# Kernel tuning notes

Hardware: AMD Instinct MI355X
Metric: run time of the kernel (lower is better)

The kernel has to match this reference:

```python
import jax, jax.numpy as jnp
import numpy as np
import math

B, NV, L = 64, 21, 2048
PATCH, STRIDE = 16, 8
PNUM = (L - PATCH) // STRIDE + 1  # 255 patches
D, H, NDIM = 128, 256, 2
PRED = 96
EPS = 1e-5
SCALE = 1.0 / math.sqrt(NDIM)  # MultiHeadEMA scale = sqrt(1/ndim)
# patch gather indices: [PNUM, PATCH]
PIDX = np.arange(PNUM)[:, None] * STRIDE + np.arange(PATCH)[None, :]


def setup_inputs() -> dict:
    key = jax.random.key(0)
    ks = jax.random.split(key, 24)
    nrm = lambda k, shape, std: std * jax.random.normal(k, shape, jnp.float32)
    inp = {}
    inp['x'] = jax.random.normal(ks[0], (B, NV, L), jnp.float32)
    # LEMencoder feature_projection: LEMblock(PATCH -> H -> D)
    inp['fp_w1'] = nrm(ks[1], (PATCH, H), 0.1)
    inp['fp_b1'] = jnp.zeros((H,), jnp.float32)
    inp['fp_w2'] = nrm(ks[2], (H, D), 0.1)
    inp['fp_b2'] = jnp.zeros((D,), jnp.float32)
    inp['fp_wr'] = nrm(ks[3], (PATCH, D), 0.1)
    inp['fp_br'] = jnp.zeros((D,), jnp.float32)
    inp['fp_g'] = jnp.ones((D,), jnp.float32)
    inp['fp_be'] = jnp.zeros((D,), jnp.float32)
    # 2 stacked encoder LEMblocks (D -> D -> D), leading layer axis
    inp['enc_w1'] = nrm(ks[4], (2, D, D), 0.05)
    inp['enc_b1'] = jnp.zeros((2, D), jnp.float32)
    inp['enc_w2'] = nrm(ks[5], (2, D, D), 0.05)
    inp['enc_b2'] = jnp.zeros((2, D), jnp.float32)
    inp['enc_wr'] = nrm(ks[6], (2, D, D), 0.05)
    inp['enc_br'] = jnp.zeros((2, D), jnp.float32)
    inp['enc_g'] = jnp.ones((2, D), jnp.float32)
    inp['enc_be'] = jnp.zeros((2, D), jnp.float32)
    # MultiHeadEMA params (unidirectional: kernel_dim == D)
    inp['ema_delta'] = nrm(ks[7], (D, NDIM, 1), 0.2)
    inp['ema_alpha'] = nrm(ks[8], (D, NDIM, 1), 0.2)
    val = jnp.array([1.0, -1.0], jnp.float32).reshape(1, NDIM, 1)  # +1/-1 alternating init
    inp['ema_beta'] = nrm(ks[9], (D, NDIM, 1), 0.02) + val
    inp['ema_gamma'] = nrm(ks[10], (D, NDIM), 1.0)
    inp['ema_omega'] = nrm(ks[11], (D,), 1.0)
    # Flatten_Head (shared): Linear(D*PNUM -> PRED)
    inp['head_w'] = nrm(ks[12], (D * PNUM, PRED), 0.02)
    inp['head_b'] = jnp.zeros((PRED,), jnp.float32)
    return inp


def _lemblock(x, w1, b1, w2, b2, wr, br, g, be):
    h = jax.nn.relu(x @ w1 + b1) @ w2 + b2
    y = h + (x @ wr + br)
    mu = jnp.mean(y, axis=-1, keepdims=True)
    var = jnp.mean(jnp.square(y - mu), axis=-1, keepdims=True)
    return g * (y - mu) * jax.lax.rsqrt(var + EPS) + be


def reference(x, fp_w1, fp_b1, fp_w2, fp_b2, fp_wr, fp_br, fp_g, fp_be,
              enc_w1, enc_b1, enc_w2, enc_b2, enc_wr, enc_br, enc_g, enc_be,
              ema_delta, ema_alpha, ema_beta, ema_gamma, ema_omega,
              head_w, head_b):
    # patching: [B, NV, L] -> [B*NV, PNUM, PATCH]
    z = x[:, :, PIDX].reshape(B * NV, PNUM, PATCH)
    # LEMencoder
    z = _lemblock(z, fp_w1, fp_b1, fp_w2, fp_b2, fp_wr, fp_br, fp_g, fp_be)
    for i in range(enc_w1.shape[0]):
        z = _lemblock(z, enc_w1[i], enc_b1[i], enc_w2[i], enc_b2[i],
                      enc_wr[i], enc_br[i], enc_g[i], enc_be[i])
    # MultiHeadEMA over patch (time) axis; input [Time=PNUM, Batch=B*NV, Channel=D]
    t = jnp.transpose(z, (1, 0, 2))
    residual = t * ema_omega
    xc = jnp.transpose(t, (1, 2, 0))  # [BN, D, PNUM]
    p = jax.nn.sigmoid(ema_delta)           # [D, N, 1]
    q = 1.0 - p * jax.nn.sigmoid(ema_alpha)  # [D, N, 1]
    vander = jnp.arange(PNUM, dtype=jnp.float32)[None, None, :] * jnp.log(q)  # [D, N, PNUM]
    kern = p * ema_beta * jnp.exp(vander)
    k = jnp.einsum('dnl,dn->dl', kern, ema_gamma * SCALE)  # [D, PNUM]
    n2 = 2 * PNUM
    out = jnp.fft.irfft(jnp.fft.rfft(xc, n=n2) * jnp.fft.rfft(k, n=n2), n=n2)[..., :PNUM]
    out = jax.nn.silu(jnp.transpose(out, (2, 0, 1)) + residual)  # [PNUM, BN, D]
    # Flatten_Head (shared): [B, NV, D, PNUM] -> flatten(-2) -> linear
    u = jnp.transpose(out, (1, 2, 0)).reshape(B, NV, D * PNUM)
    return u @ head_w + head_b  # [B, NV, PRED]
```

## Files before the change

### kernel.cpp

```cpp
#include <hip/hip_runtime.h>

typedef unsigned short u16;
typedef short bf8v __attribute__((ext_vector_type(8)));
typedef float f4v __attribute__((ext_vector_type(4)));
typedef float f16v __attribute__((ext_vector_type(16)));

#define DEV static __device__ __forceinline__

constexpr int BB   = 64;
constexpr int NV   = 21;
constexpr int BN   = BB * NV;
constexpr int PNUM = 255;
constexpr int D    = 128;
constexpr int PRED = 96;
constexpr int ROWS = BN * PNUM;
constexpr int KH   = D * PNUM;
constexpr int CH   = 30;
constexpr int KPC  = KH / CH;
constexpr int HITER = KPC / 32;
constexpr float EMA_SCALE = 0.70710678118654752440f;

DEV float bf2f(u16 h) { return __uint_as_float(((unsigned)h) << 16); }
DEV u16 f2bf(float f) {
  unsigned u = __float_as_uint(f);
  return (u16)((u + 0x7fffu + ((u >> 16) & 1u)) >> 16);
}
DEV unsigned pkbf2(float a, float b) {
  unsigned ua = __float_as_uint(a) + 0x8000u;
  unsigned ub = __float_as_uint(b) + 0x8000u;
  return __builtin_amdgcn_perm(ub, ua, 0x07060302u);
}
DEV bf8v mk4(unsigned a, unsigned b, unsigned c, unsigned d) {
  int4 t = {(int)a, (int)b, (int)c, (int)d};
  bf8v r;
  __builtin_memcpy(&r, &t, 16);
  return r;
}
DEV bf8v ld8(const u16* p) {
  bf8v r;
  __builtin_memcpy(&r, p, 16);
  return r;
}
DEV f4v mfma16(bf8v a, bf8v b, f4v c) {
  return __builtin_amdgcn_mfma_f32_16x16x32_bf16(a, b, c, 0, 0, 0);
}
DEV f16v mfma32(bf8v a, bf8v b, f16v c) {
  return __builtin_amdgcn_mfma_f32_32x32x16_bf16(a, b, c, 0, 0, 0);
}
DEV f16v zero16() {
  f16v r;
#pragma unroll
  for (int i = 0; i < 16; i++) r[i] = 0.f;
  return r;
}

#define FRG(pk, ks)                                                            \
  mk4(pk[(ks) >> 1][2 * ((ks) & 1)][0], pk[(ks) >> 1][2 * ((ks) & 1)][1],      \
      pk[(ks) >> 1][2 * ((ks) & 1) + 1][0], pk[(ks) >> 1][2 * ((ks) & 1) + 1][1])

__global__ void swz_all(
    const float* __restrict__ fw1, const float* __restrict__ fw2,
    const float* __restrict__ fwr, const float* __restrict__ ew1,
    const float* __restrict__ ew2, const float* __restrict__ ewr,
    const float* __restrict__ hw, u16* __restrict__ wb, u16* __restrict__ wsh) {
  int b = blockIdx.x;
  if (b >= 560) {
    int i = (b - 560) * 256 + threadIdx.x;
    if (i >= KH * PRED) return;
    int kp = i / PRED, n = i - kp * PRED;
    int l = kp >> 7, d = kp & 127;
    wsh[((size_t)(kp >> 3) * PRED + n) * 8 + (kp & 7)] =
        f2bf(hw[(size_t)(d * PNUM + l) * PRED + n]);
    return;
  }
  const float* src; u16* dst; int K, N, Kp;
  if (b < 32)       { src = fw1; dst = wb;          K = 16;  N = 256; Kp = 32; }
  else if (b < 160) { b -= 32;  src = fw2; dst = wb + 8192;  K = 256; N = 128; Kp = 256; }
  else if (b < 176) { b -= 160; src = fwr; dst = wb + 40960; K = 16;  N = 128; Kp = 32; }
  else {
    int e = (b - 176) >> 6; b = (b - 176) & 63;
    int l = e / 3, w = e - 3 * l;
    const float* basep = (w == 0) ? ew1 : (w == 1) ? ew2 : ewr;
    src = basep + (size_t)l * 16384;
    dst = wb + 45056 + e * 16384;
    K = 128; N = 128; Kp = 128;
  }
  int i = b * 256 + threadIdx.x;
  if (i >= Kp * N) return;
  int k = i / N, n = i - k * N;
  int np = (n & ~12) | ((n & 4) << 1) | ((n & 8) >> 1);
  u16 v = (k < K) ? f2bf(src[(size_t)k * N + np]) : (u16)0;
  dst[((size_t)(k >> 3) * N + n) * 8 + (k & 7)] = v;
}

__global__ __launch_bounds__(128, 2) void k_lem(
    const float* __restrict__ x,
    const u16* __restrict__ ws1, const float* __restrict__ b1,
    const u16* __restrict__ ws2, const u16* __restrict__ wsr,
    const float* __restrict__ b2, const float* __restrict__ br,
    const float* __restrict__ g, const float* __restrict__ be,
    const u16* __restrict__ wse, const float* __restrict__ eb1,
    const float* __restrict__ eb2, const float* __restrict__ ebr,
    const float* __restrict__ eg, const float* __restrict__ ebe,
    u16* __restrict__ zout) {
  __shared__ __align__(16) u16 zst[64 * 132];
  const int t = threadIdx.x;
  const int lane = t & 63, w = t >> 6;
  const int hh = lane >> 5, r5 = lane & 31;
  const int tile = blockIdx.x;
  const int row = tile * 64 + w * 32 + r5;

  bf8v azv;
  {
    unsigned R = (unsigned)row;
    unsigned bn = R / 255u;
    unsigned p = R - bn * 255u;
    const float* px = x + (size_t)bn * 2048u + p * 8u + hh * 8;
    float4 v0 = *(const float4*)px;
    float4 v1 = *(const float4*)(px + 4);
    azv = mk4(pkbf2(v0.x, v0.y), pkbf2(v0.z, v0.w),
              pkbf2(v1.x, v1.y), pkbf2(v1.z, v1.w));
  }

  unsigned hpk[8][4][2];
  unsigned zpk[4][4][2];

#pragma unroll
  for (int half = 0; half < 2; half++) {
    f16v a[4];
#pragma unroll
    for (int gg = 0; gg < 4; gg++) {
      bf8v wf = ld8(ws1 + ((size_t)(hh * 256 + (half * 4 + gg) * 32 + r5)) * 8);
      a[gg] = mfma32(wf, azv, zero16());
    }
#pragma unroll
    for (int gg = 0; gg < 4; gg++)
#pragma unroll
      for (int wq = 0; wq < 4; wq++) {
        int c0 = (half * 4 + gg) * 32 + ((wq >> 1) << 4) + ((wq & 1) << 2) + (hh << 3);
        float4 bv = *(const float4*)(b1 + c0);
        float v0 = fmaxf(a[gg][wq * 4 + 0] + bv.x, 0.f);
        float v1 = fmaxf(a[gg][wq * 4 + 1] + bv.y, 0.f);
        float v2 = fmaxf(a[gg][wq * 4 + 2] + bv.z, 0.f);
        float v3 = fmaxf(a[gg][wq * 4 + 3] + bv.w, 0.f);
        hpk[half * 4 + gg][wq][0] = pkbf2(v0, v1);
        hpk[half * 4 + gg][wq][1] = pkbf2(v2, v3);
      }
  }

  f16v acc[4];
  {
    bf8v wq[3][4];
#pragma unroll
    for (int b = 0; b < 2; b++)
#pragma unroll
      for (int gg = 0; gg < 4; gg++)
        wq[b][gg] = ld8(ws2 + ((size_t)((2 * b + hh) * 128 + gg * 32 + r5)) * 8);
    {
      bf8v wr4[4];
#pragma unroll
      for (int gg = 0; gg < 4; gg++)
        wr4[gg] = ld8(wsr + ((size_t)(hh * 128 + gg * 32 + r5)) * 8);
#pragma unroll
      for (int gg = 0; gg < 4; gg++) acc[gg] = mfma32(wr4[gg], azv, zero16());
    }
#pragma unroll
    for (int u = 0; u < 16; u++) {
      if (u + 2 < 16) {
#pragma unroll
        for (int gg = 0; gg < 4; gg++)
          wq[(u + 2) % 3][gg] =
              ld8(ws2 + ((size_t)((2 * (u + 2) + hh) * 128 + gg * 32 + r5)) * 8);
      }
      bf8v bfr = FRG(hpk, u);
#pragma unroll
      for (int gg = 0; gg < 4; gg++) acc[gg] = mfma32(wq[u % 3][gg], bfr, acc[gg]);
    }
    float s = 0.f, s2 = 0.f;
#pragma unroll
    for (int gg = 0; gg < 4; gg++)
#pragma unroll
      for (int wq4 = 0; wq4 < 4; wq4++) {
        int c0 = gg * 32 + ((wq4 >> 1) << 4) + ((wq4 & 1) << 2) + (hh << 3);
        float4 bv2 = *(const float4*)(b2 + c0);
        float4 bvr = *(const float4*)(br + c0);
        acc[gg][wq4 * 4 + 0] += bv2.x + bvr.x;
        acc[gg][wq4 * 4 + 1] += bv2.y + bvr.y;
        acc[gg][wq4 * 4 + 2] += bv2.z + bvr.z;
        acc[gg][wq4 * 4 + 3] += bv2.w + bvr.w;
#pragma unroll
        for (int sidx = 0; sidx < 4; sidx++) {
          float v = acc[gg][wq4 * 4 + sidx];
          s += v; s2 += v * v;
        }
      }
    s += __shfl_xor(s, 32, 64); s2 += __shfl_xor(s2, 32, 64);
    float mean = s * (1.f / 128.f);
    float rstd = rsqrtf(s2 * (1.f / 128.f) - mean * mean + 1e-5f);
#pragma unroll
    for (int gg = 0; gg < 4; gg++)
#pragma unroll
      for (int wq4 = 0; wq4 < 4; wq4++) {
        int c0 = gg * 32 + ((wq4 >> 1) << 4) + ((wq4 & 1) << 2) + (hh << 3);
        float4 gv = *(const float4*)(g + c0);
        float4 bv = *(const float4*)(be + c0);
        float v0 = (acc[gg][wq4 * 4 + 0] - mean) * rstd * gv.x + bv.x;
        float v1 = (acc[gg][wq4 * 4 + 1] - mean) * rstd * gv.y + bv.y;
        float v2 = (acc[gg][wq4 * 4 + 2] - mean) * rstd * gv.z + bv.z;
        float v3 = (acc[gg][wq4 * 4 + 3] - mean) * rstd * gv.w + bv.w;
        zpk[gg][wq4][0] = pkbf2(v0, v1);
        zpk[gg][wq4][1] = pkbf2(v2, v3);
      }
  }

#pragma unroll 1
  for (int L = 0; L < 2; L++) {
    const u16* w1p = wse + (size_t)(L * 3 + 0) * 16384;
    const u16* w2p = wse + (size_t)(L * 3 + 1) * 16384;
    const u16* wrp = wse + (size_t)(L * 3 + 2) * 16384;
    unsigned hp2[4][4][2];
    {
      f16v a2[4];
#pragma unroll
      for (int gg = 0; gg < 4; gg++) a2[gg] = zero16();
      bf8v wq[3][4];
#pragma unroll
      for (int b = 0; b < 2; b++)
#pragma unroll
        for (int gg = 0; gg < 4; gg++)
          wq[b][gg] = ld8(w1p + ((size_t)((2 * b + hh) * 128 + gg * 32 + r5)) * 8);
#pragma unroll
      for (int u = 0; u < 8; u++) {
        if (u + 2 < 8) {
#pragma unroll
          for (int gg = 0; gg < 4; gg++)
            wq[(u + 2) % 3][gg] =
                ld8(w1p + ((size_t)((2 * (u + 2) + hh) * 128 + gg * 32 + r5)) * 8);
        }
        bf8v bfr = FRG(zpk, u);
#pragma unroll
        for (int gg = 0; gg < 4; gg++) a2[gg] = mfma32(wq[u % 3][gg], bfr, a2[gg]);
      }
#pragma unroll
      for (int gg = 0; gg < 4; gg++)
#pragma unroll
        for (int wq4 = 0; wq4 < 4; wq4++) {
          int c0 = gg * 32 + ((wq4 >> 1) << 4) + ((wq4 & 1) << 2) + (hh << 3);
          float4 bv = *(const float4*)(eb1 + L * 128 + c0);
          float v0 = fmaxf(a2[gg][wq4 * 4 + 0] + bv.x, 0.f);
          float v1 = fmaxf(a2[gg][wq4 * 4 + 1] + bv.y, 0.f);
          float v2 = fmaxf(a2[gg][wq4 * 4 + 2] + bv.z, 0.f);
          float v3 = fmaxf(a2[gg][wq4 * 4 + 3] + bv.w, 0.f);
          hp2[gg][wq4][0] = pkbf2(v0, v1);
          hp2[gg][wq4][1] = pkbf2(v2, v3);
        }
    }
#pragma unroll
    for (int gg = 0; gg < 4; gg++) acc[gg] = zero16();
    {
      bf8v wq[3][4];
#pragma unroll
      for (int b = 0; b < 2; b++)
#pragma unroll
        for (int gg = 0; gg < 4; gg++)
          wq[b][gg] = ld8(w2p + ((size_t)((2 * b + hh) * 128 + gg * 32 + r5)) * 8);
#pragma unroll
      for (int u = 0; u < 16; u++) {
        if (u + 2 < 16) {
          int v = u + 2;
          const u16* wp = (v < 8) ? w2p : wrp;
          int kg = v & 7;
#pragma unroll
          for (int gg = 0; gg < 4; gg++)
            wq[v % 3][gg] = ld8(wp + ((size_t)((2 * kg + hh) * 128 + gg * 32 + r5)) * 8);
        }
        bf8v bfr = (u < 8) ? FRG(hp2, u) : FRG(zpk, (u - 8));
#pragma unroll
        for (int gg = 0; gg < 4; gg++) acc[gg] = mfma32(wq[u % 3][gg], bfr, acc[gg]);
      }
    }
    float s = 0.f, s2 = 0.f;
#pragma unroll
    for (int gg = 0; gg < 4; gg++)
#pragma unroll
      for (int wq4 = 0; wq4 < 4; wq4++) {
        int c0 = gg * 32 + ((wq4 >> 1) << 4) + ((wq4 & 1) << 2) + (hh << 3);
        float4 bv2 = *(const float4*)(eb2 + L * 128 + c0);
        float4 bvr = *(const float4*)(ebr + L * 128 + c0);
        acc[gg][wq4 * 4 + 0] += bv2.x + bvr.x;
        acc[gg][wq4 * 4 + 1] += bv2.y + bvr.y;
        acc[gg][wq4 * 4 + 2] += bv2.z + bvr.z;
        acc[gg][wq4 * 4 + 3] += bv2.w + bvr.w;
#pragma unroll
        for (int sidx = 0; sidx < 4; sidx++) {
          float v = acc[gg][wq4 * 4 + sidx];
          s += v; s2 += v * v;
        }
      }
    s += __shfl_xor(s, 32, 64); s2 += __shfl_xor(s2, 32, 64);
    float mean = s * (1.f / 128.f);
    float rstd = rsqrtf(s2 * (1.f / 128.f) - mean * mean + 1e-5f);
#pragma unroll
    for (int gg = 0; gg < 4; gg++)
#pragma unroll
      for (int wq4 = 0; wq4 < 4; wq4++) {
        int c0 = gg * 32 + ((wq4 >> 1) << 4) + ((wq4 & 1) << 2) + (hh << 3);
        float4 gv = *(const float4*)(eg + L * 128 + c0);
        float4 bv = *(const float4*)(ebe + L * 128 + c0);
        float v0 = (acc[gg][wq4 * 4 + 0] - mean) * rstd * gv.x + bv.x;
        float v1 = (acc[gg][wq4 * 4 + 1] - mean) * rstd * gv.y + bv.y;
        float v2 = (acc[gg][wq4 * 4 + 2] - mean) * rstd * gv.z + bv.z;
        float v3 = (acc[gg][wq4 * 4 + 3] - mean) * rstd * gv.w + bv.w;
        unsigned plo = pkbf2(v0, v1), phi = pkbf2(v2, v3);
        if (L == 0) {
          zpk[gg][wq4][0] = plo;
          zpk[gg][wq4][1] = phi;
        } else {
          uint2 pv = {plo, phi};
          *(uint2*)(zst + (w * 32 + r5) * 132 + c0) = pv;
        }
      }
  }

#pragma unroll
  for (int it = 0; it < 8; it++) {
    int lu = it * 64 + lane;
    int rr = lu >> 4, seg = lu & 15;
    int orow = w * 32 + rr;
    *(uint4*)(zout + ((size_t)tile * 64 + orow) * 128 + seg * 8) =
        *(const uint4*)(zst + orow * 132 + seg * 8);
  }
}

__global__ __launch_bounds__(128) void k_ema(
    u16* __restrict__ z,
    const float* __restrict__ pdel, const float* __restrict__ palp,
    const float* __restrict__ pbet, const float* __restrict__ pgam,
    const float* __restrict__ pome) {
  __shared__ __align__(16) u16 zc[64 * 128];
  const int t = threadIdx.x;
  const int bn = blockIdx.x;
  float p0 = 1.f / (1.f + __expf(-pdel[t * 2 + 0]));
  float p1 = 1.f / (1.f + __expf(-pdel[t * 2 + 1]));
  float q0 = 1.f - p0 / (1.f + __expf(-palp[t * 2 + 0]));
  float q1 = 1.f - p1 / (1.f + __expf(-palp[t * 2 + 1]));
  float w0 = p0 * pbet[t * 2 + 0] * pgam[t * 2 + 0] * EMA_SCALE;
  float w1 = p1 * pbet[t * 2 + 1] * pgam[t * 2 + 1] * EMA_SCALE;
  float om = pome[t];
  float s0 = 0.f, s1 = 0.f;
  u16* slab = z + (size_t)bn * KH;

  for (int ch = 0; ch < 4; ch++) {
    int nrow = (ch < 3) ? 64 : 63;
    int nval = nrow * 128;
    for (int i = t * 8; i < nval; i += 128 * 8)
      *(uint4*)(zc + i) = *(const uint4*)(slab + ch * 8192 + i);
    __syncthreads();
    for (int j0 = 0; j0 < nrow; j0 += 8) {
      float xs[8];
#pragma unroll
      for (int jj = 0; jj < 8; jj++)
        if (j0 + jj < nrow) xs[jj] = bf2f(zc[(j0 + jj) * 128 + t]);
#pragma unroll
      for (int jj = 0; jj < 8; jj++)
        if (j0 + jj < nrow) {
          float xv = xs[jj];
          s0 = q0 * s0 + xv;
          s1 = q1 * s1 + xv;
          float v = w0 * s0 + w1 * s1 + om * xv;
          xs[jj] = v / (1.f + __expf(-v));
        }
#pragma unroll
      for (int jj = 0; jj < 8; jj++)
        if (j0 + jj < nrow)
          zc[(j0 + jj) * 128 + t] = (u16)((__float_as_uint(xs[jj]) + 0x8000u) >> 16);
    }
    __syncthreads();
    for (int i = t * 8; i < nval; i += 128 * 8)
      *(uint4*)(slab + ch * 8192 + i) = *(const uint4*)(zc + i);
    __syncthreads();
  }
}

__global__ __launch_bounds__(256) void k_head(
    const u16* __restrict__ u, const u16* __restrict__ whs, float* __restrict__ part) {
  const int t = threadIdx.x;
  const int lane = t & 63, wid = t >> 6;
  const int quad = lane >> 4, lc = lane & 15;
  const int tile = blockIdx.x;
  const int ch = blockIdx.y;
  const int m0 = tile * 64 + wid * 16;
  const u16* Ab = u + (size_t)(m0 + lc) * KH + (size_t)ch * KPC;
  const int g0 = ch * (KPC / 8);
  f4v acc[6];
#pragma unroll
  for (int n = 0; n < 6; n++) acc[n] = (f4v){0.f, 0.f, 0.f, 0.f};
  bf8v a_nxt = ld8(Ab + quad * 8);
  bf8v b_nxt[6];
#pragma unroll
  for (int n = 0; n < 6; n++)
    b_nxt[n] = ld8(whs + ((size_t)(g0 + quad) * PRED + n * 16 + lc) * 8);
  for (int ks = 0; ks < HITER; ks++) {
    bf8v a_cur = a_nxt;
    bf8v b_cur[6];
#pragma unroll
    for (int n = 0; n < 6; n++) b_cur[n] = b_nxt[n];
    if (ks < HITER - 1) {
      a_nxt = ld8(Ab + (ks + 1) * 32 + quad * 8);
#pragma unroll
      for (int n = 0; n < 6; n++)
        b_nxt[n] = ld8(whs + ((size_t)(g0 + (ks + 1) * 4 + quad) * PRED + n * 16 + lc) * 8);
    }
#pragma unroll
    for (int n = 0; n < 6; n++) acc[n] = mfma16(a_cur, b_cur[n], acc[n]);
  }
#pragma unroll
  for (int n = 0; n < 6; n++) {
    int col = n * 16 + lc;
#pragma unroll
    for (int r = 0; r < 4; r++)
      part[((size_t)ch * BN + m0 + quad * 4 + r) * PRED + col] = acc[n][r];
  }
}

__global__ __launch_bounds__(256) void k_red(
    const float* __restrict__ part, const float* __restrict__ hb, float* __restrict__ out) {
  int i = blockIdx.x * 256 + threadIdx.x;
  if (i >= BN * PRED) return;
  int row = i / PRED, col = i - row * PRED;
  float s = hb[col];
#pragma unroll 5
  for (int c = 0; c < CH; c++) s += part[((size_t)c * BN + row) * PRED + col];
  out[i] = s;
}

extern "C" void kernel_launch(void* const* d_in, const int* in_sizes, int n_in,
                              void* d_out, int out_size, void* d_ws, size_t ws_size,
                              hipStream_t stream) {
  const float* x      = (const float*)d_in[0];
  const float* fp_w1  = (const float*)d_in[1];
  const float* fp_b1  = (const float*)d_in[2];
  const float* fp_w2  = (const float*)d_in[3];
  const float* fp_b2  = (const float*)d_in[4];
  const float* fp_wr  = (const float*)d_in[5];
  const float* fp_br  = (const float*)d_in[6];
  const float* fp_g   = (const float*)d_in[7];
  const float* fp_be  = (const float*)d_in[8];
  const float* enc_w1 = (const float*)d_in[9];
  const float* enc_b1 = (const float*)d_in[10];
  const float* enc_w2 = (const float*)d_in[11];
  const float* enc_b2 = (const float*)d_in[12];
  const float* enc_wr = (const float*)d_in[13];
  const float* enc_br = (const float*)d_in[14];
  const float* enc_g  = (const float*)d_in[15];
  const float* enc_be = (const float*)d_in[16];
  const float* e_del  = (const float*)d_in[17];
  const float* e_alp  = (const float*)d_in[18];
  const float* e_bet  = (const float*)d_in[19];
  const float* e_gam  = (const float*)d_in[20];
  const float* e_om   = (const float*)d_in[21];
  const float* head_w = (const float*)d_in[22];
  const float* head_b = (const float*)d_in[23];

  char* base = (char*)d_ws;
  u16* z3 = (u16*)base;
  const size_t EZB = (size_t)ROWS * 128 * 2;
  float* part = (float*)(base + EZB);
  const size_t PARTB = (size_t)CH * BN * PRED * 4;
  u16* wb = (u16*)(base + EZB + PARTB);
  u16* ws1 = wb;
  u16* ws2 = wb + 8192;
  u16* wsr = wb + 40960;
  u16* wse = wb + 45056;
  u16* wsh = wb + 143360;

  swz_all<<<560 + (KH * PRED + 255) / 256, 256, 0, stream>>>(
      fp_w1, fp_w2, fp_wr, enc_w1, enc_w2, enc_wr, head_w, wb, wsh);

  k_lem<<<ROWS / 64, 128, 0, stream>>>(x, ws1, fp_b1, ws2, wsr, fp_b2, fp_br, fp_g, fp_be,
                                       wse, enc_b1, enc_b2, enc_br, enc_g, enc_be, z3);
  k_ema<<<BN, 128, 0, stream>>>(z3, e_del, e_alp, e_bet, e_gam, e_om);
  k_head<<<dim3(21, CH), 256, 0, stream>>>(z3, wsh, part);
  k_red<<<(BN * PRED + 255) / 256, 256, 0, stream>>>(part, head_b, (float*)d_out);
}
```

Before: 408.6 us.

## Stream hidden layer through MFMA chain to cut registers in k_lem, raise occupancy

The first LEM block no longer holds the whole 256-wide hidden activation in registers. Each 32-column slice of the hidden layer is computed and immediately fed into the second GEMM, with the weight loads double-buffered. In the encoder layers the hidden activations are staged through per-row shared memory instead of register arrays. The weight prefetch ring drops from three buffers to two, and launch bounds move from 2 to 3 blocks per SIMD. The aim is lower VGPR pressure for more waves in flight, at the cost of extra LDS traffic and a shallower prefetch depth.

```diff
diff --git a/kernel.cpp b/kernel.cpp
--- a/kernel.cpp
+++ b/kernel.cpp
@@ -18,6 +18,7 @@
 constexpr int CH   = 30;
 constexpr int KPC  = KH / CH;
 constexpr int HITER = KPC / 32;
+constexpr int LSTR = 132;
 constexpr float EMA_SCALE = 0.70710678118654752440f;
 
 DEV float bf2f(u16 h) { return __uint_as_float(((unsigned)h) << 16); }
@@ -93,7 +94,7 @@
   dst[((size_t)(k >> 3) * N + n) * 8 + (k & 7)] = v;
 }
 
-__global__ __launch_bounds__(128, 2) void k_lem(
+__global__ __launch_bounds__(128, 3) void k_lem(
     const float* __restrict__ x,
     const u16* __restrict__ ws1, const float* __restrict__ b1,
     const u16* __restrict__ ws2, const u16* __restrict__ wsr,
@@ -103,12 +104,13 @@
     const float* __restrict__ eb2, const float* __restrict__ ebr,
     const float* __restrict__ eg, const float* __restrict__ ebe,
     u16* __restrict__ zout) {
-  __shared__ __align__(16) u16 zst[64 * 132];
+  __shared__ __align__(16) u16 zst[64 * LSTR];
   const int t = threadIdx.x;
   const int lane = t & 63, w = t >> 6;
   const int hh = lane >> 5, r5 = lane & 31;
   const int tile = blockIdx.x;
   const int row = tile * 64 + w * 32 + r5;
+  u16* zrow = zst + (w * 32 + r5) * LSTR;
 
   bf8v azv;
   {
@@ -122,77 +124,75 @@
               pkbf2(v1.x, v1.y), pkbf2(v1.z, v1.w));
   }
 
-  unsigned hpk[8][4][2];
+  f16v acc[4];
   unsigned zpk[4][4][2];
 
-#pragma unroll
-  for (int half = 0; half < 2; half++) {
-    f16v a[4];
-#pragma unroll
-    for (int gg = 0; gg < 4; gg++) {
-      bf8v wf = ld8(ws1 + ((size_t)(hh * 256 + (half * 4 + gg) * 32 + r5)) * 8);
-      a[gg] = mfma32(wf, azv, zero16());
-    }
+  {
+    bf8v wr4[4];
 #pragma unroll
     for (int gg = 0; gg < 4; gg++)
+      wr4[gg] = ld8(wsr + ((size_t)(hh * 128 + gg * 32 + r5)) * 8);
+#pragma unroll
+    for (int gg = 0; gg < 4; gg++) acc[gg] = mfma32(wr4[gg], azv, zero16());
+  }
+
+  {
+    bf8v w2b[2][8];
+    bf8v w1c = ld8(ws1 + ((size_t)(hh * 256 + r5)) * 8);
+#pragma unroll
+    for (int q = 0; q < 8; q++) {
+      int gg2 = q >> 1, kk = q & 1;
+      w2b[0][q] = ld8(ws2 + ((size_t)((2 * kk + hh) * 128 + gg2 * 32 + r5)) * 8);
+    }
+#pragma unroll
+    for (int gg = 0; gg < 8; gg++) {
+      int cur = gg & 1;
+      f16v a = mfma32(w1c, azv, zero16());
+      if (gg < 7) {
+        w1c = ld8(ws1 + ((size_t)(hh * 256 + (gg + 1) * 32 + r5)) * 8);
+#pragma unroll
+        for (int q = 0; q < 8; q++) {
+          int gg2 = q >> 1, kk = q & 1;
+          w2b[cur ^ 1][q] =
+              ld8(ws2 + ((size_t)((4 * (gg + 1) + 2 * kk + hh) * 128 + gg2 * 32 + r5)) * 8);
+        }
+      }
+      unsigned pk[4][2];
 #pragma unroll
       for (int wq = 0; wq < 4; wq++) {
-        int c0 = (half * 4 + gg) * 32 + ((wq >> 1) << 4) + ((wq & 1) << 2) + (hh << 3);
+        int c0 = gg * 32 + ((wq >> 1) << 4) + ((wq & 1) << 2) + (hh << 3);
         float4 bv = *(const float4*)(b1 + c0);
-        float v0 = fmaxf(a[gg][wq * 4 + 0] + bv.x, 0.f);
-        float v1 = fmaxf(a[gg][wq * 4 + 1] + bv.y, 0.f);
-        float v2 = fmaxf(a[gg][wq * 4 + 2] + bv.z, 0.f);
-        float v3 = fmaxf(a[gg][wq * 4 + 3] + bv.w, 0.f);
-        hpk[half * 4 + gg][wq][0] = pkbf2(v0, v1);
-        hpk[half * 4 + gg][wq][1] = pkbf2(v2, v3);
-      }
-  }
-
-  f16v acc[4];
+        float v0 = fmaxf(a[wq * 4 + 0] + bv.x, 0.f);
+        float v1 = fmaxf(a[wq * 4 + 1] + bv.y, 0.f);
+        float v2 = fmaxf(a[wq * 4 + 2] + bv.z, 0.f);
+        float v3 = fmaxf(a[wq * 4 + 3] + bv.w, 0.f);
+        pk[wq][0] = pkbf2(v0, v1);
+        pk[wq][1] = pkbf2(v2, v3);
+      }
+      bf8v fr0 = mk4(pk[0][0], pk[0][1], pk[1][0], pk[1][1]);
+      bf8v fr1 = mk4(pk[2][0], pk[2][1], pk[3][0], pk[3][1]);
+#pragma unroll
+      for (int gg2 = 0; gg2 < 4; gg2++) {
+        acc[gg2] = mfma32(w2b[cur][gg2 * 2 + 0], fr0, acc[gg2]);
+        acc[gg2] = mfma32(w2b[cur][gg2 * 2 + 1], fr1, acc[gg2]);
+      }
+    }
+  }
   {
-    bf8v wq[3][4];
-#pragma unroll
-    for (int b = 0; b < 2; b++)
-#pragma unroll
-      for (int gg = 0; gg < 4; gg++)
-        wq[b][gg] = ld8(ws2 + ((size_t)((2 * b + hh) * 128 + gg * 32 + r5)) * 8);
-    {
-      bf8v wr4[4];
-#pragma unroll
-      for (int gg = 0; gg < 4; gg++)
-        wr4[gg] = ld8(wsr + ((size_t)(hh * 128 + gg * 32 + r5)) * 8);
-#pragma unroll
-      for (int gg = 0; gg < 4; gg++) acc[gg] = mfma32(wr4[gg], azv, zero16());
-    }
-#pragma unroll
-    for (int u = 0; u < 16; u++) {
-      if (u + 2 < 16) {
-#pragma unroll
-        for (int gg = 0; gg < 4; gg++)
-          wq[(u + 2) % 3][gg] =
-              ld8(ws2 + ((size_t)((2 * (u + 2) + hh) * 128 + gg * 32 + r5)) * 8);
-      }
-      bf8v bfr = FRG(hpk, u);
-#pragma unroll
-      for (int gg = 0; gg < 4; gg++) acc[gg] = mfma32(wq[u % 3][gg], bfr, acc[gg]);
-    }
     float s = 0.f, s2 = 0.f;
 #pragma unroll
     for (int gg = 0; gg < 4; gg++)
 #pragma unroll
-      for (int wq4 = 0; wq4 < 4; wq4++) {
-        int c0 = gg * 32 + ((wq4 >> 1) << 4) + ((wq4 & 1) << 2) + (hh << 3);
+      for (int wq = 0; wq < 4; wq++) {
+        int c0 = gg * 32 + ((wq >> 1) << 4) + ((wq & 1) << 2) + (hh << 3);
         float4 bv2 = *(const float4*)(b2 + c0);
         float4 bvr = *(const float4*)(br + c0);
-        acc[gg][wq4 * 4 + 0] += bv2.x + bvr.x;
-        acc[gg][wq4 * 4 + 1] += bv2.y + bvr.y;
-        acc[gg][wq4 * 4 + 2] += bv2.z + bvr.z;
-        acc[gg][wq4 * 4 + 3] += bv2.w + bvr.w;
-#pragma unroll
-        for (int sidx = 0; sidx < 4; sidx++) {
-          float v = acc[gg][wq4 * 4 + sidx];
-          s += v; s2 += v * v;
-        }
+        acc[gg][wq * 4 + 0] += bv2.x + bvr.x;
+        acc[gg][wq * 4 + 1] += bv2.y + bvr.y;
+        acc[gg][wq * 4 + 2] += bv2.z + bvr.z;
+        acc[gg][wq * 4 + 3] += bv2.w + bvr.w;
+#pragma unroll
+        for (int i = 0; i < 4; i++) { float v = acc[gg][wq * 4 + i]; s += v; s2 += v * v; }
       }
     s += __shfl_xor(s, 32, 64); s2 += __shfl_xor(s2, 32, 64);
     float mean = s * (1.f / 128.f);
@@ -200,16 +200,16 @@
 #pragma unroll
     for (int gg = 0; gg < 4; gg++)
 #pragma unroll
-      for (int wq4 = 0; wq4 < 4; wq4++) {
-        int c0 = gg * 32 + ((wq4 >> 1) << 4) + ((wq4 & 1) << 2) + (hh << 3);
+      for (int wq = 0; wq < 4; wq++) {
+        int c0 = gg * 32 + ((wq >> 1) << 4) + ((wq & 1) << 2) + (hh << 3);
         float4 gv = *(const float4*)(g + c0);
         float4 bv = *(const float4*)(be + c0);
-        float v0 = (acc[gg][wq4 * 4 + 0] - mean) * rstd * gv.x + bv.x;
-        float v1 = (acc[gg][wq4 * 4 + 1] - mean) * rstd * gv.y + bv.y;
-        float v2 = (acc[gg][wq4 * 4 + 2] - mean) * rstd * gv.z + bv.z;
-        float v3 = (acc[gg][wq4 * 4 + 3] - mean) * rstd * gv.w + bv.w;
-        zpk[gg][wq4][0] = pkbf2(v0, v1);
-        zpk[gg][wq4][1] = pkbf2(v2, v3);
+        float v0 = (acc[gg][wq * 4 + 0] - mean) * rstd * gv.x + bv.x;
+        float v1 = (acc[gg][wq * 4 + 1] - mean) * rstd * gv.y + bv.y;
+        float v2 = (acc[gg][wq * 4 + 2] - mean) * rstd * gv.z + bv.z;
+        float v3 = (acc[gg][wq * 4 + 3] - mean) * rstd * gv.w + bv.w;
+        zpk[gg][wq][0] = pkbf2(v0, v1);
+        zpk[gg][wq][1] = pkbf2(v2, v3);
       }
   }
 
@@ -218,84 +218,91 @@
     const u16* w1p = wse + (size_t)(L * 3 + 0) * 16384;
     const u16* w2p = wse + (size_t)(L * 3 + 1) * 16384;
     const u16* wrp = wse + (size_t)(L * 3 + 2) * 16384;
-    unsigned hp2[4][4][2];
     {
       f16v a2[4];
 #pragma unroll
       for (int gg = 0; gg < 4; gg++) a2[gg] = zero16();
-      bf8v wq[3][4];
-#pragma unroll
-      for (int b = 0; b < 2; b++)
-#pragma unroll
-        for (int gg = 0; gg < 4; gg++)
-          wq[b][gg] = ld8(w1p + ((size_t)((2 * b + hh) * 128 + gg * 32 + r5)) * 8);
+      bf8v wqb[2][4];
+#pragma unroll
+      for (int gg = 0; gg < 4; gg++)
+        wqb[0][gg] = ld8(w1p + ((size_t)(hh * 128 + gg * 32 + r5)) * 8);
 #pragma unroll
       for (int u = 0; u < 8; u++) {
-        if (u + 2 < 8) {
+        int cur = u & 1;
+        if (u < 7) {
 #pragma unroll
           for (int gg = 0; gg < 4; gg++)
-            wq[(u + 2) % 3][gg] =
-                ld8(w1p + ((size_t)((2 * (u + 2) + hh) * 128 + gg * 32 + r5)) * 8);
+            wqb[cur ^ 1][gg] =
+                ld8(w1p + ((size_t)((2 * (u + 1) + hh) * 128 + gg * 32 + r5)) * 8);
         }
         bf8v bfr = FRG(zpk, u);
 #pragma unroll
-        for (int gg = 0; gg < 4; gg++) a2[gg] = mfma32(wq[u % 3][gg], bfr, a2[gg]);
-      }
-#pragma unroll
-      for (int gg = 0; gg < 4; gg++)
-#pragma unroll
-        for (int wq4 = 0; wq4 < 4; wq4++) {
-          int c0 = gg * 32 + ((wq4 >> 1) << 4) + ((wq4 & 1) << 2) + (hh << 3);
+        for (int gg = 0; gg < 4; gg++) a2[gg] = mfma32(wqb[cur][gg], bfr, a2[gg]);
+      }
+#pragma unroll
+      for (int gg = 0; gg < 4; gg++) {
+        unsigned pk[4][2];
+#pragma unroll
+        for (int wq = 0; wq < 4; wq++) {
+          int c0 = gg * 32 + ((wq >> 1) << 4) + ((wq & 1) << 2) + (hh << 3);
           float4 bv = *(const float4*)(eb1 + L * 128 + c0);
-          float v0 = fmaxf(a2[gg][wq4 * 4 + 0] + bv.x, 0.f);
-          float v1 = fmaxf(a2[gg][wq4 * 4 + 1] + bv.y, 0.f);
-          float v2 = fmaxf(a2[gg][wq4 * 4 + 2] + bv.z, 0.f);
-          float v3 = fmaxf(a2[gg][wq4 * 4 + 3] + bv.w, 0.f);
-          hp2[gg][wq4][0] = pkbf2(v0, v1);
-          hp2[gg][wq4][1] = pkbf2(v2, v3);
-        }
+          float v0 = fmaxf(a2[gg][wq * 4 + 0] + bv.x, 0.f);
+          float v1 = fmaxf(a2[gg][wq * 4 + 1] + bv.y, 0.f);
+          float v2 = fmaxf(a2[gg][wq * 4 + 2] + bv.z, 0.f);
+          float v3 = fmaxf(a2[gg][wq * 4 + 3] + bv.w, 0.f);
+          pk[wq][0] = pkbf2(v0, v1);
+          pk[wq][1] = pkbf2(v2, v3);
+        }
+        uint2 p0 = {pk[0][0], pk[0][1]};
+        uint2 p1 = {pk[1][0], pk[1][1]};
+        uint2 p2 = {pk[2][0], pk[2][1]};
+        uint2 p3 = {pk[3][0], pk[3][1]};
+        *(uint2*)(zrow + gg * 32 + (hh << 3) + 0) = p0;
+        *(uint2*)(zrow + gg * 32 + (hh << 3) + 4) = p1;
+        *(uint2*)(zrow + gg * 32 + 16 + (hh << 3) + 0) = p2;
+        *(uint2*)(zrow + gg * 32 + 16 + (hh << 3) + 4) = p3;
+      }
     }
 #pragma unroll
     for (int gg = 0; gg < 4; gg++) acc[gg] = zero16();
     {
-      bf8v wq[3][4];
-#pragma unroll
-      for (int b = 0; b < 2; b++)
-#pragma unroll
-        for (int gg = 0; gg < 4; gg++)
-          wq[b][gg] = ld8(w2p + ((size_t)((2 * b + hh) * 128 + gg * 32 + r5)) * 8);
+      bf8v wqb[2][4];
+      bf8v hf[2];
+#pragma unroll
+      for (int gg = 0; gg < 4; gg++)
+        wqb[0][gg] = ld8(w2p + ((size_t)(hh * 128 + gg * 32 + r5)) * 8);
+      hf[0] = ld8(zrow + (hh << 3));
 #pragma unroll
       for (int u = 0; u < 16; u++) {
-        if (u + 2 < 16) {
-          int v = u + 2;
+        int cur = u & 1;
+        if (u + 1 < 16) {
+          int v = u + 1;
           const u16* wp = (v < 8) ? w2p : wrp;
           int kg = v & 7;
 #pragma unroll
           for (int gg = 0; gg < 4; gg++)
-            wq[v % 3][gg] = ld8(wp + ((size_t)((2 * kg + hh) * 128 + gg * 32 + r5)) * 8);
-        }
-        bf8v bfr = (u < 8) ? FRG(hp2, u) : FRG(zpk, (u - 8));
-#pragma unroll
-        for (int gg = 0; gg < 4; gg++) acc[gg] = mfma32(wq[u % 3][gg], bfr, acc[gg]);
+            wqb[cur ^ 1][gg] = ld8(wp + ((size_t)((2 * kg + hh) * 128 + gg * 32 + r5)) * 8);
+          if (v < 8) hf[cur ^ 1] = ld8(zrow + v * 16 + (hh << 3));
+        }
+        bf8v bfr = (u < 8) ? hf[cur] : FRG(zpk, (u - 8));
+#pragma unroll
+        for (int gg = 0; gg < 4; gg++) acc[gg] = mfma32(wqb[cur][gg], bfr, acc[gg]);
       }
     }
     float s = 0.f, s2 = 0.f;
 #pragma unroll
     for (int gg = 0; gg < 4; gg++)
 #pragma unroll
-      for (int wq4 = 0; wq4 < 4; wq4++) {
-        int c0 = gg * 32 + ((wq4 >> 1) << 4) + ((wq4 & 1) << 2) + (hh << 3);
+      for (int wq = 0; wq < 4; wq++) {
+        int c0 = gg * 32 + ((wq >> 1) << 4) + ((wq & 1) << 2) + (hh << 3);
         float4 bv2 = *(const float4*)(eb2 + L * 128 + c0);
         float4 bvr = *(const float4*)(ebr + L * 128 + c0);
-        acc[gg][wq4 * 4 + 0] += bv2.x + bvr.x;
-        acc[gg][wq4 * 4 + 1] += bv2.y + bvr.y;
-        acc[gg][wq4 * 4 + 2] += bv2.z + bvr.z;
-        acc[gg][wq4 * 4 + 3] += bv2.w + bvr.w;
-#pragma unroll
-        for (int sidx = 0; sidx < 4; sidx++) {
-          float v = acc[gg][wq4 * 4 + sidx];
-          s += v; s2 += v * v;
-        }
+        acc[gg][wq * 4 + 0] += bv2.x + bvr.x;
+        acc[gg][wq * 4 + 1] += bv2.y + bvr.y;
+        acc[gg][wq * 4 + 2] += bv2.z + bvr.z;
+        acc[gg][wq * 4 + 3] += bv2.w + bvr.w;
+#pragma unroll
+        for (int i = 0; i < 4; i++) { float v = acc[gg][wq * 4 + i]; s += v; s2 += v * v; }
       }
     s += __shfl_xor(s, 32, 64); s2 += __shfl_xor(s2, 32, 64);
     float mean = s * (1.f / 128.f);
@@ -303,21 +310,21 @@
 #pragma unroll
     for (int gg = 0; gg < 4; gg++)
 #pragma unroll
-      for (int wq4 = 0; wq4 < 4; wq4++) {
-        int c0 = gg * 32 + ((wq4 >> 1) << 4) + ((wq4 & 1) << 2) + (hh << 3);
+      for (int wq = 0; wq < 4; wq++) {
+        int c0 = gg * 32 + ((wq >> 1) << 4) + ((wq & 1) << 2) + (hh << 3);
         float4 gv = *(const float4*)(eg + L * 128 + c0);
         float4 bv = *(const float4*)(ebe + L * 128 + c0);
-        float v0 = (acc[gg][wq4 * 4 + 0] - mean) * rstd * gv.x + bv.x;
-        float v1 = (acc[gg][wq4 * 4 + 1] - mean) * rstd * gv.y + bv.y;
-        float v2 = (acc[gg][wq4 * 4 + 2] - mean) * rstd * gv.z + bv.z;
-        float v3 = (acc[gg][wq4 * 4 + 3] - mean) * rstd * gv.w + bv.w;
+        float v0 = (acc[gg][wq * 4 + 0] - mean) * rstd * gv.x + bv.x;
+        float v1 = (acc[gg][wq * 4 + 1] - mean) * rstd * gv.y + bv.y;
+        float v2 = (acc[gg][wq * 4 + 2] - mean) * rstd * gv.z + bv.z;
+        float v3 = (acc[gg][wq * 4 + 3] - mean) * rstd * gv.w + bv.w;
         unsigned plo = pkbf2(v0, v1), phi = pkbf2(v2, v3);
         if (L == 0) {
-          zpk[gg][wq4][0] = plo;
-          zpk[gg][wq4][1] = phi;
+          zpk[gg][wq][0] = plo;
+          zpk[gg][wq][1] = phi;
         } else {
           uint2 pv = {plo, phi};
-          *(uint2*)(zst + (w * 32 + r5) * 132 + c0) = pv;
+          *(uint2*)(zrow + c0) = pv;
         }
       }
   }
@@ -328,7 +335,7 @@
     int rr = lu >> 4, seg = lu & 15;
     int orow = w * 32 + rr;
     *(uint4*)(zout + ((size_t)tile * 64 + orow) * 128 + seg * 8) =
-        *(const uint4*)(zst + orow * 132 + seg * 8);
+        *(const uint4*)(zst + orow * LSTR + seg * 8);
   }
 }
 
```

After: 515.4 us. 26.1% more time.
